# Kernel optimization log

Measured on AMD Instinct MI355X. Metric: run time of the kernel, lower is better.

The kernel has to match this reference:

```python
import jax, jax.numpy as jnp
import numpy as np

B, C_IN, N, T = 16, 2, 207, 12
E = 1863
EMB = 64
HEADS = 8
F_DIM = EMB * T  # 768


def setup_inputs() -> dict:
    key = jax.random.key(0)
    ks = jax.random.split(key, 12)
    s = 0.05
    x = jax.random.normal(ks[0], (B, C_IN, N, T), jnp.float32)
    src = jax.random.randint(ks[1], (E,), 0, N)
    dst = jax.random.randint(ks[2], (E,), 0, N)
    # ensure every node has an incoming edge (self loops in the tail)
    loop = jnp.arange(N)
    src = src.at[-N:].set(loop)
    dst = dst.at[-N:].set(loop)
    Ws = jax.random.normal(ks[3], (EMB, C_IN), jnp.float32) * s
    bs = jnp.zeros((EMB,), jnp.float32)
    Wc = jax.random.normal(ks[4], (EMB, C_IN), jnp.float32) * s
    bc = jnp.zeros((EMB,), jnp.float32)
    W1 = jax.random.normal(ks[5], (F_DIM, HEADS * F_DIM), jnp.float32) * s
    al1 = jax.random.normal(ks[6], (HEADS, F_DIM), jnp.float32) * s
    ar1 = jax.random.normal(ks[7], (HEADS, F_DIM), jnp.float32) * s
    b1 = jnp.zeros((HEADS, F_DIM), jnp.float32)
    W2 = jax.random.normal(ks[8], (F_DIM, HEADS * F_DIM), jnp.float32) * s
    al2 = jax.random.normal(ks[9], (HEADS, F_DIM), jnp.float32) * s
    ar2 = jax.random.normal(ks[10], (HEADS, F_DIM), jnp.float32) * s
    b2 = jnp.zeros((HEADS, F_DIM), jnp.float32)
    return dict(x=x, src=src, dst=dst, Ws=Ws, bs=bs, Wc=Wc, bc=bc,
                W1=W1, al1=al1, ar1=ar1, b1=b1, W2=W2, al2=al2, ar2=ar2, b2=b2)


def _gat_layer(h, W, al, ar, b, src, dst):
    # h: [B, N, F]  (dropout disabled: eval-mode reference)
    feat = (h @ W).reshape(B, N, HEADS, F_DIM)          # [B,N,H,F]
    el = jnp.einsum('bnhf,hf->bnh', feat, al)           # src scores
    er = jnp.einsum('bnhf,hf->bnh', feat, ar)           # dst scores
    e = jax.nn.leaky_relu(el[:, src] + er[:, dst], 0.2)  # [B,E,H]

    def edge_softmax(ev):  # ev: [E,H], softmax over edges sharing a dst node
        m = jax.ops.segment_max(ev, dst, num_segments=N)
        ex = jnp.exp(ev - m[dst])
        denom = jax.ops.segment_sum(ex, dst, num_segments=N)
        return ex / denom[dst]

    alpha = jax.vmap(edge_softmax)(e)                   # [B,E,H]
    msg = alpha[..., None] * feat[:, src]               # [B,E,H,F]
    rst = jax.vmap(lambda m_: jax.ops.segment_sum(m_, dst, num_segments=N))(msg)
    rst = jax.nn.elu(rst + b)                            # bias + F.elu activation
    return rst.mean(axis=2)                              # mean over heads -> [B,N,F]


def reference(x, src, dst, Ws, bs, Wc, bc, W1, al1, ar1, b1, W2, al2, ar2, b2):
    # 1x1 convs == channel matmuls
    x1 = jnp.einsum('bcnt,oc->bont', x, Ws) + bs[None, :, None, None]
    x2 = jax.nn.leaky_relu(jnp.einsum('bcnt,oc->bont', x, Wc) + bc[None, :, None, None], 0.01)
    xm = x1 + x2                                         # [B,EMB,N,T]
    h = xm.transpose(0, 2, 1, 3).reshape(B, N, F_DIM)    # [B,N,768]
    h = _gat_layer(h, W1, al1, ar1, b1, src, dst)
    h = _gat_layer(h, W2, al2, ar2, b2, src, dst)
    gc = h.reshape(B, N, EMB, T).transpose(0, 2, 1, 3)   # [B,EMB,N,T]
    return xm + gc
```

## Files before the change

### kernel.cpp

```cpp
#include <hip/hip_runtime.h>

#define BB 16
#define NNODE 207
#define TTS 12
#define NE 1863
#define NEP2 1920
#define NH 8
#define FD 768
#define HFD 6144
#define MM 3312
#define MP 3328

typedef short bf16x8 __attribute__((ext_vector_type(8)));
typedef float f32x4 __attribute__((ext_vector_type(4)));

typedef __attribute__((address_space(3))) unsigned int lds_u32;
typedef __attribute__((address_space(1))) const unsigned int glb_u32;

__device__ __forceinline__ unsigned short f2b(float f) {
    unsigned int u = __float_as_uint(f);
    u = (u + 0x7FFFu + ((u >> 16) & 1u)) >> 16;
    return (unsigned short)u;
}
__device__ __forceinline__ float b2f(unsigned short b) {
    return __uint_as_float(((unsigned int)b) << 16);
}

__global__ __launch_bounds__(256) void transpose_w(const float* __restrict__ W,
                                                   unsigned short* __restrict__ Wt) {
    __shared__ float tile[64][65];
    const int k0 = blockIdx.x * 64;
    const int n0 = blockIdx.y * 64;
    const int c = threadIdx.x & 63, r0 = threadIdx.x >> 6;
#pragma unroll
    for (int i = 0; i < 16; i++) {
        int r = r0 + i * 4;
        tile[r][c] = W[(size_t)(k0 + r) * HFD + n0 + c];
    }
    __syncthreads();
#pragma unroll
    for (int i = 0; i < 16; i++) {
        int r = r0 + i * 4;
        Wt[(size_t)(n0 + r) * FD + k0 + c] = f2b(tile[c][r]);
    }
}

__global__ __launch_bounds__(256) void prep_h(const float* __restrict__ x,
                                              const float* __restrict__ Ws, const float* __restrict__ bs,
                                              const float* __restrict__ Wc, const float* __restrict__ bc,
                                              float* __restrict__ h0, unsigned short* __restrict__ hbf) {
    const int bn = blockIdx.x;
    const int t = threadIdx.x;
    if (bn >= MM) {
#pragma unroll
        for (int c = 0; c < 3; c++) hbf[(size_t)bn * FD + c * 256 + t] = 0;
        return;
    }
    const int b = bn / NNODE, n = bn % NNODE;
#pragma unroll
    for (int c = 0; c < 3; c++) {
        int idx = c * 256 + t;
        int e = idx / TTS, tt = idx % TTS;
        float x0 = x[((size_t)(b * 2 + 0) * NNODE + n) * TTS + tt];
        float x1 = x[((size_t)(b * 2 + 1) * NNODE + n) * TTS + tt];
        float s1 = Ws[e * 2] * x0 + Ws[e * 2 + 1] * x1 + bs[e];
        float s2 = Wc[e * 2] * x0 + Wc[e * 2 + 1] * x1 + bc[e];
        s2 = s2 > 0.f ? s2 : 0.01f * s2;
        float v = s1 + s2;
        h0[(size_t)bn * FD + idx] = v;
        hbf[(size_t)bn * FD + idx] = f2b(v);
    }
}

#define CSR_EBLK 468
__global__ __launch_bounds__(256) void build_csr3(const int* __restrict__ dst,
                                                  int* __restrict__ ptr, int* __restrict__ cidx) {
    __shared__ int dl[NEP2];
    const int t = threadIdx.x;
    const int wv = t >> 6, lane = t & 63;
    for (int i = t; i < NEP2; i += 256) dl[i] = (i < NE) ? dst[i] : 0x0FFFFFFF;
    __syncthreads();
    if (blockIdx.x < CSR_EBLK) {
        const int e = blockIdx.x * 4 + wv;
        if (e >= NE) return;
        const int d = dl[e];
        int pos = 0;
#pragma unroll
        for (int j = 0; j < 30; j++) {
            int i = lane + j * 64;
            int di = dl[i];
            pos += (int)(di < d) + (int)((i < e) & (di == d));
        }
#pragma unroll
        for (int off = 32; off > 0; off >>= 1) pos += __shfl_down(pos, off);
        if (lane == 0) cidx[pos] = e;
    } else {
        const int n = (blockIdx.x - CSR_EBLK) * 4 + wv;
        if (n > NNODE) return;
        int cnt = 0;
#pragma unroll
        for (int j = 0; j < 30; j++) cnt += (int)(dl[lane + j * 64] < n);
#pragma unroll
        for (int off = 32; off > 0; off >>= 1) cnt += __shfl_down(cnt, off);
        if (lane == 0) ptr[n] = cnt;
    }
}

__global__ __launch_bounds__(256) void gemm_bf16(const unsigned short* __restrict__ A,
                                                 const unsigned short* __restrict__ Bt,
                                                 unsigned short* __restrict__ C) {
    __shared__ __align__(16) unsigned short Alds[128 * 32];
    __shared__ __align__(16) unsigned short Blds[128 * 32];
    const int t = threadIdx.x;
    const int lane = t & 63;
    const int wv = t >> 6;
    const int wr = (wv >> 1) * 64, wc = (wv & 1) * 64;
    const int mt = blockIdx.y * 128, nt = blockIdx.x * 128;
    const int lm = lane & 15;
    const int kb = (lane >> 4) * 8;

    const int r0 = (wv * 2) * 16 + (lane >> 2);
    const int r1 = (wv * 2 + 1) * 16 + (lane >> 2);
    const int cseg = (lane & 3) * 8;
    const size_t aoff0 = (size_t)(mt + r0) * FD + cseg;
    const size_t aoff1 = (size_t)(mt + r1) * FD + cseg;
    const size_t boff0 = (size_t)(nt + r0) * FD + cseg;
    const size_t boff1 = (size_t)(nt + r1) * FD + cseg;
    unsigned short* la0 = Alds + (size_t)(wv * 2) * 512;
    unsigned short* la1 = Alds + (size_t)(wv * 2 + 1) * 512;
    unsigned short* lb0 = Blds + (size_t)(wv * 2) * 512;
    unsigned short* lb1 = Blds + (size_t)(wv * 2 + 1) * 512;

    f32x4 acc[4][4] = {};
    for (int ks = 0; ks < FD; ks += 32) {
        __builtin_amdgcn_global_load_lds((glb_u32*)(A + aoff0 + ks), (lds_u32*)la0, 16, 0, 0);
        __builtin_amdgcn_global_load_lds((glb_u32*)(A + aoff1 + ks), (lds_u32*)la1, 16, 0, 0);
        __builtin_amdgcn_global_load_lds((glb_u32*)(Bt + boff0 + ks), (lds_u32*)lb0, 16, 0, 0);
        __builtin_amdgcn_global_load_lds((glb_u32*)(Bt + boff1 + ks), (lds_u32*)lb1, 16, 0, 0);
        __syncthreads();
        bf16x8 af[4], bfv[4];
#pragma unroll
        for (int i = 0; i < 4; i++) af[i] = *(const bf16x8*)(Alds + (wr + i * 16 + lm) * 32 + kb);
#pragma unroll
        for (int j = 0; j < 4; j++) bfv[j] = *(const bf16x8*)(Blds + (wc + j * 16 + lm) * 32 + kb);
#pragma unroll
        for (int i = 0; i < 4; i++)
#pragma unroll
            for (int j = 0; j < 4; j++)
                acc[i][j] = __builtin_amdgcn_mfma_f32_16x16x32_bf16(af[i], bfv[j], acc[i][j], 0, 0, 0);
        __syncthreads();
    }
    const int rbase = (lane >> 4) * 4;
#pragma unroll
    for (int i = 0; i < 4; i++) {
#pragma unroll
        for (int r = 0; r < 4; r++) {
            int grow = mt + wr + i * 16 + rbase + r;
            if (grow < MM) {
#pragma unroll
                for (int j = 0; j < 4; j++) {
                    int gcol = nt + wc + j * 16 + lm;
                    C[(size_t)grow * HFD + gcol] = f2b(acc[i][j][r]);
                }
            }
        }
    }
}

__global__ __launch_bounds__(256) void eler(const unsigned short* __restrict__ feat,
                                            const float* __restrict__ al, const float* __restrict__ ar,
                                            float* __restrict__ el, float* __restrict__ er) {
    const int p = blockIdx.x * 4 + (threadIdx.x >> 6);
    const int lane = threadIdx.x & 63;
    const int bn = p >> 3, hh = p & 7;
    const size_t base = (size_t)bn * HFD + hh * FD;
    float sl = 0.f, sr = 0.f;
#pragma unroll
    for (int j = 0; j < 12; j++) {
        int f = lane + j * 64;
        float fv = b2f(feat[base + f]);
        sl += fv * al[hh * FD + f];
        sr += fv * ar[hh * FD + f];
    }
#pragma unroll
    for (int off = 32; off > 0; off >>= 1) {
        sl += __shfl_down(sl, off);
        sr += __shfl_down(sr, off);
    }
    if (lane == 0) {
        el[bn * NH + hh] = sl;
        er[bn * NH + hh] = sr;
    }
}

__global__ __launch_bounds__(256) void edge_softmax(const float* __restrict__ el, const float* __restrict__ er,
                                                    const int* __restrict__ cptr, const int* __restrict__ cidx,
                                                    const int* __restrict__ src, float* __restrict__ alp) {
    const int t = blockIdx.x * 256 + threadIdx.x;
    if (t >= BB * NNODE * NH) return;
    const int hh = t & 7;
    const int n = (t >> 3) % NNODE;
    const int b = t / (NNODE * NH);
    const float erv = er[(b * NNODE + n) * NH + hh];
    const int p0 = cptr[n], p1 = cptr[n + 1];
    float m = -1e30f;
    for (int j = p0; j < p1; j++) {
        int e = cidx[j];
        float s = el[(b * NNODE + src[e]) * NH + hh] + erv;
        s = s > 0.f ? s : 0.2f * s;
        m = fmaxf(m, s);
    }
    float den = 0.f;
    for (int j = p0; j < p1; j++) {
        int e = cidx[j];
        float s = el[(b * NNODE + src[e]) * NH + hh] + erv;
        s = s > 0.f ? s : 0.2f * s;
        float ex = expf(s - m);
        den += ex;
        alp[((size_t)b * NE + e) * NH + hh] = ex;
    }
    const float inv = 1.f / den;
    for (int j = p0; j < p1; j++) {
        int e = cidx[j];
        alp[((size_t)b * NE + e) * NH + hh] *= inv;
    }
}

template <int LAST>
__global__ __launch_bounds__(256) void msg_agg(const unsigned short* __restrict__ feat,
                                               const float* __restrict__ alp,
                                               const int* __restrict__ cptr, const int* __restrict__ cidx,
                                               const int* __restrict__ src, const float* __restrict__ bias,
                                               unsigned short* __restrict__ hbf_out,
                                               const float* __restrict__ h0, float* __restrict__ out) {
    __shared__ float rstl[HFD];
    __shared__ int src_l[32];
    __shared__ float alph[32][NH];
    const int bn = (blockIdx.x & 7) * (MM / 8) + (blockIdx.x >> 3);
    const int b = bn / NNODE, n = bn % NNODE;
    const int t = threadIdx.x;
    const int h0i = t / 96, h1i = (256 + t) / 96, h2i = (512 + t) / 96;
    float acc[3][8] = {};
    const int p0 = cptr[n], p1 = cptr[n + 1];
    for (int base = p0; base < p1; base += 32) {
        const int cnt = min(32, p1 - base);
        if (t < cnt) src_l[t] = src[cidx[base + t]];
        {
            int j = t >> 3, hh = t & 7;
            if (j < cnt) alph[j][hh] = alp[((size_t)b * NE + cidx[base + j]) * NH + hh];
        }
        __syncthreads();
        for (int j2 = 0; j2 < cnt; j2++) {
            const size_t srow = (size_t)(b * NNODE + src_l[j2]) * HFD;
            const float a0 = alph[j2][h0i], a1 = alph[j2][h1i], a2 = alph[j2][h2i];
            uint4 pk;
            unsigned int w;
            pk = *(const uint4*)(feat + srow + (size_t)(0 * 256 + t) * 8);
            w = pk.x; acc[0][0] += a0 * b2f((unsigned short)w); acc[0][1] += a0 * b2f((unsigned short)(w >> 16));
            w = pk.y; acc[0][2] += a0 * b2f((unsigned short)w); acc[0][3] += a0 * b2f((unsigned short)(w >> 16));
            w = pk.z; acc[0][4] += a0 * b2f((unsigned short)w); acc[0][5] += a0 * b2f((unsigned short)(w >> 16));
            w = pk.w; acc[0][6] += a0 * b2f((unsigned short)w); acc[0][7] += a0 * b2f((unsigned short)(w >> 16));
            pk = *(const uint4*)(feat + srow + (size_t)(1 * 256 + t) * 8);
            w = pk.x; acc[1][0] += a1 * b2f((unsigned short)w); acc[1][1] += a1 * b2f((unsigned short)(w >> 16));
            w = pk.y; acc[1][2] += a1 * b2f((unsigned short)w); acc[1][3] += a1 * b2f((unsigned short)(w >> 16));
            w = pk.z; acc[1][4] += a1 * b2f((unsigned short)w); acc[1][5] += a1 * b2f((unsigned short)(w >> 16));
            w = pk.w; acc[1][6] += a1 * b2f((unsigned short)w); acc[1][7] += a1 * b2f((unsigned short)(w >> 16));
            pk = *(const uint4*)(feat + srow + (size_t)(2 * 256 + t) * 8);
            w = pk.x; acc[2][0] += a2 * b2f((unsigned short)w); acc[2][1] += a2 * b2f((unsigned short)(w >> 16));
            w = pk.y; acc[2][2] += a2 * b2f((unsigned short)w); acc[2][3] += a2 * b2f((unsigned short)(w >> 16));
            w = pk.z; acc[2][4] += a2 * b2f((unsigned short)w); acc[2][5] += a2 * b2f((unsigned short)(w >> 16));
            w = pk.w; acc[2][6] += a2 * b2f((unsigned short)w); acc[2][7] += a2 * b2f((unsigned short)(w >> 16));
        }
        __syncthreads();
    }
#pragma unroll
    for (int c = 0; c < 3; c++) {
        int v = c * 256 + t;
#pragma unroll
        for (int u = 0; u < 8; u++) rstl[v * 8 + u] = acc[c][u];
    }
    __syncthreads();
#pragma unroll
    for (int q = 0; q < 3; q++) {
        int f = q * 256 + t;
        float val = 0.f;
#pragma unroll
        for (int hh = 0; hh < 8; hh++) {
            float r = rstl[hh * FD + f] + bias[hh * FD + f];
            val += (r > 0.f) ? r : (expf(r) - 1.f);
        }
        val *= 0.125f;
        if (LAST) {
            int e_ = f / TTS, tt_ = f % TTS;
            out[((size_t)(b * 64 + e_) * NNODE + n) * TTS + tt_] = h0[(size_t)bn * FD + f] + val;
        } else {
            hbf_out[(size_t)bn * FD + f] = f2b(val);
        }
    }
}

extern "C" void kernel_launch(void* const* d_in, const int* in_sizes, int n_in,
                              void* d_out, int out_size, void* d_ws, size_t ws_size,
                              hipStream_t stream) {
    const float* x = (const float*)d_in[0];
    const int* src = (const int*)d_in[1];
    const int* dst = (const int*)d_in[2];
    const float* Ws = (const float*)d_in[3];
    const float* bs = (const float*)d_in[4];
    const float* Wc = (const float*)d_in[5];
    const float* bc = (const float*)d_in[6];
    const float* W1 = (const float*)d_in[7];
    const float* al1 = (const float*)d_in[8];
    const float* ar1 = (const float*)d_in[9];
    const float* b1 = (const float*)d_in[10];
    const float* W2 = (const float*)d_in[11];
    const float* al2 = (const float*)d_in[12];
    const float* ar2 = (const float*)d_in[13];
    const float* b2 = (const float*)d_in[14];
    float* out = (float*)d_out;

    char* w = (char*)d_ws;
    size_t off = 0;
    auto alloc = [&](size_t bytes) -> void* {
        void* p = w + off;
        off = (off + bytes + 255) & ~(size_t)255;
        return p;
    };
    float* h0 = (float*)alloc((size_t)MM * FD * 4);
    unsigned short* hbf = (unsigned short*)alloc((size_t)MP * FD * 2);
    unsigned short* Wt = (unsigned short*)alloc((size_t)HFD * FD * 2);
    unsigned short* feat = (unsigned short*)alloc((size_t)MM * HFD * 2);
    float* el = (float*)alloc((size_t)MM * NH * 4);
    float* er = (float*)alloc((size_t)MM * NH * 4);
    float* alp = (float*)alloc((size_t)BB * NE * NH * 4);
    int* cptr = (int*)alloc((NNODE + 1) * 4);
    int* cidx = (int*)alloc(NE * 4);

    transpose_w<<<dim3(12, 96), 256, 0, stream>>>(W1, Wt);
    prep_h<<<MP, 256, 0, stream>>>(x, Ws, bs, Wc, bc, h0, hbf);
    build_csr3<<<CSR_EBLK + 52, 256, 0, stream>>>(dst, cptr, cidx);

    gemm_bf16<<<dim3(48, 26), 256, 0, stream>>>(hbf, Wt, feat);
    transpose_w<<<dim3(12, 96), 256, 0, stream>>>(W2, Wt);
    eler<<<6624, 256, 0, stream>>>(feat, al1, ar1, el, er);
    edge_softmax<<<104, 256, 0, stream>>>(el, er, cptr, cidx, src, alp);
    msg_agg<0><<<MM, 256, 0, stream>>>(feat, alp, cptr, cidx, src, b1, hbf, nullptr, nullptr);

    gemm_bf16<<<dim3(48, 26), 256, 0, stream>>>(hbf, Wt, feat);
    eler<<<6624, 256, 0, stream>>>(feat, al2, ar2, el, er);
    edge_softmax<<<104, 256, 0, stream>>>(el, er, cptr, cidx, src, alp);
    msg_agg<1><<<MM, 256, 0, stream>>>(feat, alp, cptr, cidx, src, b2, nullptr, h0, out);
}
```

Baseline: 238.9 us.

## Fuse attention score projections into GEMM epilogue, swizzle LDS, remap tiles per XCD

Computes the per-head el/er dot products directly from the fp32 GEMM accumulators in the epilogue, writing per-64-column partial sums that a small reduce kernel combines. This removes the separate eler kernel, which re-read the whole bf16 feat tensor. The change also XOR-swizzles the LDS layout to cut bank conflicts and remaps the 1D block index so each XCD works on a contiguous tile region for better L2 locality. In exchange it adds epilogue shuffles and partial-sum buffers. The scores are now taken from fp32 accumulators rather than bf16-rounded features, so numerics shift slightly.

Measured after the change: 258.4 us. 8.2% more time.

```diff
diff --git a/kernel.cpp b/kernel.cpp
--- a/kernel.cpp
+++ b/kernel.cpp
@@ -108,20 +108,29 @@
 
 __global__ __launch_bounds__(256) void gemm_bf16(const unsigned short* __restrict__ A,
                                                  const unsigned short* __restrict__ Bt,
-                                                 unsigned short* __restrict__ C) {
+                                                 unsigned short* __restrict__ C,
+                                                 const float* __restrict__ al,
+                                                 const float* __restrict__ ar,
+                                                 float* __restrict__ pel,
+                                                 float* __restrict__ per) {
     __shared__ __align__(16) unsigned short Alds[128 * 32];
     __shared__ __align__(16) unsigned short Blds[128 * 32];
     const int t = threadIdx.x;
     const int lane = t & 63;
     const int wv = t >> 6;
     const int wr = (wv >> 1) * 64, wc = (wv & 1) * 64;
-    const int mt = blockIdx.y * 128, nt = blockIdx.x * 128;
+    const int id = blockIdx.x;
+    const int xcd = id & 7, k = id >> 3;
+    const int tr = (xcd & 1) * 13 + k / 12;
+    const int tc = (xcd >> 1) * 12 + k % 12;
+    const int mt = tr * 128, nt = tc * 128;
     const int lm = lane & 15;
-    const int kb = (lane >> 4) * 8;
+    const int rsw = (lm >> 1) & 3;
+    const int s4 = lane >> 4;
 
     const int r0 = (wv * 2) * 16 + (lane >> 2);
     const int r1 = (wv * 2 + 1) * 16 + (lane >> 2);
-    const int cseg = (lane & 3) * 8;
+    const int cseg = (((lane & 3) ^ ((lane >> 3) & 3)) * 8);
     const size_t aoff0 = (size_t)(mt + r0) * FD + cseg;
     const size_t aoff1 = (size_t)(mt + r1) * FD + cseg;
     const size_t boff0 = (size_t)(nt + r0) * FD + cseg;
@@ -140,9 +149,11 @@
         __syncthreads();
         bf16x8 af[4], bfv[4];
 #pragma unroll
-        for (int i = 0; i < 4; i++) af[i] = *(const bf16x8*)(Alds + (wr + i * 16 + lm) * 32 + kb);
-#pragma unroll
-        for (int j = 0; j < 4; j++) bfv[j] = *(const bf16x8*)(Blds + (wc + j * 16 + lm) * 32 + kb);
+        for (int i = 0; i < 4; i++)
+            af[i] = *(const bf16x8*)(Alds + (wr + i * 16 + lm) * 32 + (s4 ^ rsw) * 8);
+#pragma unroll
+        for (int j = 0; j < 4; j++)
+            bfv[j] = *(const bf16x8*)(Blds + (wc + j * 16 + lm) * 32 + (s4 ^ rsw) * 8);
 #pragma unroll
         for (int i = 0; i < 4; i++)
 #pragma unroll
@@ -150,7 +161,7 @@
                 acc[i][j] = __builtin_amdgcn_mfma_f32_16x16x32_bf16(af[i], bfv[j], acc[i][j], 0, 0, 0);
         __syncthreads();
     }
-    const int rbase = (lane >> 4) * 4;
+    const int rbase = s4 * 4;
 #pragma unroll
     for (int i = 0; i < 4; i++) {
 #pragma unroll
@@ -165,32 +176,52 @@
             }
         }
     }
-}
-
-__global__ __launch_bounds__(256) void eler(const unsigned short* __restrict__ feat,
-                                            const float* __restrict__ al, const float* __restrict__ ar,
-                                            float* __restrict__ el, float* __restrict__ er) {
-    const int p = blockIdx.x * 4 + (threadIdx.x >> 6);
-    const int lane = threadIdx.x & 63;
-    const int bn = p >> 3, hh = p & 7;
-    const size_t base = (size_t)bn * HFD + hh * FD;
-    float sl = 0.f, sr = 0.f;
+    float alv[4], arv[4];
+#pragma unroll
+    for (int j = 0; j < 4; j++) {
+        int gcol = nt + wc + j * 16 + lm;
+        alv[j] = al[gcol];
+        arv[j] = ar[gcol];
+    }
+    const int pidx = tc * 2 + (wc >> 6);
+#pragma unroll
+    for (int i = 0; i < 4; i++) {
+#pragma unroll
+        for (int r = 0; r < 4; r++) {
+            float pl = acc[i][0][r] * alv[0] + acc[i][1][r] * alv[1] +
+                       acc[i][2][r] * alv[2] + acc[i][3][r] * alv[3];
+            float pr = acc[i][0][r] * arv[0] + acc[i][1][r] * arv[1] +
+                       acc[i][2][r] * arv[2] + acc[i][3][r] * arv[3];
+#pragma unroll
+            for (int m = 1; m < 16; m <<= 1) {
+                pl += __shfl_xor(pl, m);
+                pr += __shfl_xor(pr, m);
+            }
+            if (lm == 0) {
+                int grow = mt + wr + i * 16 + rbase + r;
+                if (grow < MM) {
+                    pel[(size_t)pidx * MP + grow] = pl;
+                    per[(size_t)pidx * MP + grow] = pr;
+                }
+            }
+        }
+    }
+}
+
+__global__ __launch_bounds__(256) void reduce_eler(const float* __restrict__ pel,
+                                                   const float* __restrict__ per,
+                                                   float* __restrict__ el, float* __restrict__ er) {
+    const int idx = blockIdx.x * 256 + threadIdx.x;
+    if (idx >= MM * NH) return;
+    const int h = idx / MM, bn = idx % MM;
+    float s = 0.f, u = 0.f;
 #pragma unroll
     for (int j = 0; j < 12; j++) {
-        int f = lane + j * 64;
-        float fv = b2f(feat[base + f]);
-        sl += fv * al[hh * FD + f];
-        sr += fv * ar[hh * FD + f];
-    }
-#pragma unroll
-    for (int off = 32; off > 0; off >>= 1) {
-        sl += __shfl_down(sl, off);
-        sr += __shfl_down(sr, off);
-    }
-    if (lane == 0) {
-        el[bn * NH + hh] = sl;
-        er[bn * NH + hh] = sr;
-    }
+        s += pel[(size_t)(h * 12 + j) * MP + bn];
+        u += per[(size_t)(h * 12 + j) * MP + bn];
+    }
+    el[bn * NH + h] = s;
+    er[bn * NH + h] = u;
 }
 
 __global__ __launch_bounds__(256) void edge_softmax(const float* __restrict__ el, const float* __restrict__ er,
@@ -335,19 +366,21 @@
     float* alp = (float*)alloc((size_t)BB * NE * NH * 4);
     int* cptr = (int*)alloc((NNODE + 1) * 4);
     int* cidx = (int*)alloc(NE * 4);
+    float* pel = (float*)alloc((size_t)96 * MP * 4);
+    float* per = (float*)alloc((size_t)96 * MP * 4);
 
     transpose_w<<<dim3(12, 96), 256, 0, stream>>>(W1, Wt);
     prep_h<<<MP, 256, 0, stream>>>(x, Ws, bs, Wc, bc, h0, hbf);
     build_csr3<<<CSR_EBLK + 52, 256, 0, stream>>>(dst, cptr, cidx);
 
-    gemm_bf16<<<dim3(48, 26), 256, 0, stream>>>(hbf, Wt, feat);
+    gemm_bf16<<<1248, 256, 0, stream>>>(hbf, Wt, feat, al1, ar1, pel, per);
     transpose_w<<<dim3(12, 96), 256, 0, stream>>>(W2, Wt);
-    eler<<<6624, 256, 0, stream>>>(feat, al1, ar1, el, er);
+    reduce_eler<<<104, 256, 0, stream>>>(pel, per, el, er);
     edge_softmax<<<104, 256, 0, stream>>>(el, er, cptr, cidx, src, alp);
     msg_agg<0><<<MM, 256, 0, stream>>>(feat, alp, cptr, cidx, src, b1, hbf, nullptr, nullptr);
 
-    gemm_bf16<<<dim3(48, 26), 256, 0, stream>>>(hbf, Wt, feat);
-    eler<<<6624, 256, 0, stream>>>(feat, al2, ar2, el, er);
+    gemm_bf16<<<1248, 256, 0, stream>>>(hbf, Wt, feat, al2, ar2, pel, per);
+    reduce_eler<<<104, 256, 0, stream>>>(pel, per, el, er);
     edge_softmax<<<104, 256, 0, stream>>>(el, er, cptr, cidx, src, alp);
     msg_agg<1><<<MM, 256, 0, stream>>>(feat, alp, cptr, cidx, src, b2, nullptr, h0, out);
 }
```

## Double-buffer GEMM LDS tiles and XOR-swizzle to avoid bank conflicts

Applied to the files above, without the earlier changes.

The bf16 GEMM now keeps two LDS buffers for the A and B tiles and prefetches the next K-slice with global_load_lds while the MFMA loop runs on the current slice. This drops one barrier per iteration and lets global loads overlap with compute. The global source column segment and the LDS read offset are XOR-swizzled per row to reduce LDS bank conflicts on the fragment reads. LDS use doubles, and correctness now depends on the write and read swizzles matching.

Result: no change. 242.7 us (+1.6%).

```diff
diff --git a/kernel.cpp b/kernel.cpp
--- a/kernel.cpp
+++ b/kernel.cpp
@@ -109,48 +109,72 @@
 __global__ __launch_bounds__(256) void gemm_bf16(const unsigned short* __restrict__ A,
                                                  const unsigned short* __restrict__ Bt,
                                                  unsigned short* __restrict__ C) {
-    __shared__ __align__(16) unsigned short Alds[128 * 32];
-    __shared__ __align__(16) unsigned short Blds[128 * 32];
+    __shared__ __align__(16) unsigned short Alds[2][128 * 32];
+    __shared__ __align__(16) unsigned short Blds[2][128 * 32];
     const int t = threadIdx.x;
     const int lane = t & 63;
     const int wv = t >> 6;
     const int wr = (wv >> 1) * 64, wc = (wv & 1) * 64;
     const int mt = blockIdx.y * 128, nt = blockIdx.x * 128;
     const int lm = lane & 15;
-    const int kb = (lane >> 4) * 8;
+    const int rsw = (lm >> 1) & 3;
+    const int s4 = lane >> 4;
+    const int rdoff = (s4 ^ rsw) * 8;
 
     const int r0 = (wv * 2) * 16 + (lane >> 2);
     const int r1 = (wv * 2 + 1) * 16 + (lane >> 2);
-    const int cseg = (lane & 3) * 8;
-    const size_t aoff0 = (size_t)(mt + r0) * FD + cseg;
-    const size_t aoff1 = (size_t)(mt + r1) * FD + cseg;
-    const size_t boff0 = (size_t)(nt + r0) * FD + cseg;
-    const size_t boff1 = (size_t)(nt + r1) * FD + cseg;
-    unsigned short* la0 = Alds + (size_t)(wv * 2) * 512;
-    unsigned short* la1 = Alds + (size_t)(wv * 2 + 1) * 512;
-    unsigned short* lb0 = Blds + (size_t)(wv * 2) * 512;
-    unsigned short* lb1 = Blds + (size_t)(wv * 2 + 1) * 512;
+    const int cseg = (((lane & 3) ^ ((lane >> 3) & 3)) * 8);
+    const unsigned short* ap0 = A + (size_t)(mt + r0) * FD + cseg;
+    const unsigned short* ap1 = A + (size_t)(mt + r1) * FD + cseg;
+    const unsigned short* bp0 = Bt + (size_t)(nt + r0) * FD + cseg;
+    const unsigned short* bp1 = Bt + (size_t)(nt + r1) * FD + cseg;
+    const int ldoff0 = (wv * 2) * 512;
+    const int ldoff1 = (wv * 2 + 1) * 512;
 
     f32x4 acc[4][4] = {};
-    for (int ks = 0; ks < FD; ks += 32) {
-        __builtin_amdgcn_global_load_lds((glb_u32*)(A + aoff0 + ks), (lds_u32*)la0, 16, 0, 0);
-        __builtin_amdgcn_global_load_lds((glb_u32*)(A + aoff1 + ks), (lds_u32*)la1, 16, 0, 0);
-        __builtin_amdgcn_global_load_lds((glb_u32*)(Bt + boff0 + ks), (lds_u32*)lb0, 16, 0, 0);
-        __builtin_amdgcn_global_load_lds((glb_u32*)(Bt + boff1 + ks), (lds_u32*)lb1, 16, 0, 0);
-        __syncthreads();
+    __builtin_amdgcn_global_load_lds((glb_u32*)(ap0), (lds_u32*)(Alds[0] + ldoff0), 16, 0, 0);
+    __builtin_amdgcn_global_load_lds((glb_u32*)(ap1), (lds_u32*)(Alds[0] + ldoff1), 16, 0, 0);
+    __builtin_amdgcn_global_load_lds((glb_u32*)(bp0), (lds_u32*)(Blds[0] + ldoff0), 16, 0, 0);
+    __builtin_amdgcn_global_load_lds((glb_u32*)(bp1), (lds_u32*)(Blds[0] + ldoff1), 16, 0, 0);
+    __syncthreads();
+
+    int cur = 0;
+#pragma unroll 1
+    for (int ks = 32; ks < FD; ks += 32) {
+        __builtin_amdgcn_global_load_lds((glb_u32*)(ap0 + ks), (lds_u32*)(Alds[cur ^ 1] + ldoff0), 16, 0, 0);
+        __builtin_amdgcn_global_load_lds((glb_u32*)(ap1 + ks), (lds_u32*)(Alds[cur ^ 1] + ldoff1), 16, 0, 0);
+        __builtin_amdgcn_global_load_lds((glb_u32*)(bp0 + ks), (lds_u32*)(Blds[cur ^ 1] + ldoff0), 16, 0, 0);
+        __builtin_amdgcn_global_load_lds((glb_u32*)(bp1 + ks), (lds_u32*)(Blds[cur ^ 1] + ldoff1), 16, 0, 0);
         bf16x8 af[4], bfv[4];
 #pragma unroll
-        for (int i = 0; i < 4; i++) af[i] = *(const bf16x8*)(Alds + (wr + i * 16 + lm) * 32 + kb);
-#pragma unroll
-        for (int j = 0; j < 4; j++) bfv[j] = *(const bf16x8*)(Blds + (wc + j * 16 + lm) * 32 + kb);
+        for (int i = 0; i < 4; i++)
+            af[i] = *(const bf16x8*)(Alds[cur] + (wr + i * 16 + lm) * 32 + rdoff);
+#pragma unroll
+        for (int j = 0; j < 4; j++)
+            bfv[j] = *(const bf16x8*)(Blds[cur] + (wc + j * 16 + lm) * 32 + rdoff);
 #pragma unroll
         for (int i = 0; i < 4; i++)
 #pragma unroll
             for (int j = 0; j < 4; j++)
                 acc[i][j] = __builtin_amdgcn_mfma_f32_16x16x32_bf16(af[i], bfv[j], acc[i][j], 0, 0, 0);
         __syncthreads();
-    }
-    const int rbase = (lane >> 4) * 4;
+        cur ^= 1;
+    }
+    {
+        bf16x8 af[4], bfv[4];
+#pragma unroll
+        for (int i = 0; i < 4; i++)
+            af[i] = *(const bf16x8*)(Alds[cur] + (wr + i * 16 + lm) * 32 + rdoff);
+#pragma unroll
+        for (int j = 0; j < 4; j++)
+            bfv[j] = *(const bf16x8*)(Blds[cur] + (wc + j * 16 + lm) * 32 + rdoff);
+#pragma unroll
+        for (int i = 0; i < 4; i++)
+#pragma unroll
+            for (int j = 0; j < 4; j++)
+                acc[i][j] = __builtin_amdgcn_mfma_f32_16x16x32_bf16(af[i], bfv[j], acc[i][j], 0, 0, 0);
+    }
+    const int rbase = s4 * 4;
 #pragma unroll
     for (int i = 0; i < 4; i++) {
 #pragma unroll
```

## Fold attention vectors into weights and compute el/er from layer inputs

Applied to the files above, without the earlier changes.

Precomputes W·al and W·ar per head so the attention scores el/er can be computed directly from the 768-wide layer input. That work is fused into prep_h and msg_agg<0>, which removes the separate eler pass over the large bf16 feat tensor. Both weight transposes now run in one launch into two buffers, and the GEMM's LDS layout gets an XOR swizzle to reduce bank conflicts. It costs a small extra precompute kernel and extra workspace, and el/er are now computed in fp32 from h rather than from bf16-rounded feat, so the numerics change slightly.

New measurement: 301.2 us. 26.1% more time.

```diff
diff --git a/kernel.cpp b/kernel.cpp
--- a/kernel.cpp
+++ b/kernel.cpp
@@ -26,9 +26,38 @@
     return __uint_as_float(((unsigned int)b) << 16);
 }
 
-__global__ __launch_bounds__(256) void transpose_w(const float* __restrict__ W,
-                                                   unsigned short* __restrict__ Wt) {
+__global__ __launch_bounds__(256) void prep_wlr(const float* __restrict__ W1,
+                                                const float* __restrict__ al1, const float* __restrict__ ar1,
+                                                const float* __restrict__ W2,
+                                                const float* __restrict__ al2, const float* __restrict__ ar2,
+                                                float* __restrict__ wlr) {
+    const int d = blockIdx.x * 256 + threadIdx.x;
+    const int which = d / 6144;
+    const int r = d % 6144;
+    const int k = r >> 3, hh = r & 7;
+    const float* W = which ? W2 : W1;
+    const float* al = which ? al2 : al1;
+    const float* ar = which ? ar2 : ar1;
+    const float4* wp = (const float4*)(W + (size_t)k * HFD + hh * FD);
+    const float4* ap = (const float4*)(al + hh * FD);
+    const float4* rp = (const float4*)(ar + hh * FD);
+    float sl = 0.f, sr = 0.f;
+    for (int j = 0; j < 192; j++) {
+        float4 w = wp[j], a = ap[j], b = rp[j];
+        sl += w.x * a.x + w.y * a.y + w.z * a.z + w.w * a.w;
+        sr += w.x * b.x + w.y * b.y + w.z * b.z + w.w * b.w;
+    }
+    wlr[(size_t)which * 12288 + 0 + hh * FD + k] = sl;
+    wlr[(size_t)which * 12288 + 6144 + hh * FD + k] = sr;
+}
+
+__global__ __launch_bounds__(256) void transpose_w2(const float* __restrict__ W1,
+                                                    const float* __restrict__ W2,
+                                                    unsigned short* __restrict__ Wt1,
+                                                    unsigned short* __restrict__ Wt2) {
     __shared__ float tile[64][65];
+    const float* W = blockIdx.z ? W2 : W1;
+    unsigned short* Wt = blockIdx.z ? Wt2 : Wt1;
     const int k0 = blockIdx.x * 64;
     const int n0 = blockIdx.y * 64;
     const int c = threadIdx.x & 63, r0 = threadIdx.x >> 6;
@@ -48,7 +77,10 @@
 __global__ __launch_bounds__(256) void prep_h(const float* __restrict__ x,
                                               const float* __restrict__ Ws, const float* __restrict__ bs,
                                               const float* __restrict__ Wc, const float* __restrict__ bc,
-                                              float* __restrict__ h0, unsigned short* __restrict__ hbf) {
+                                              const float* __restrict__ wl, const float* __restrict__ wr,
+                                              float* __restrict__ h0, unsigned short* __restrict__ hbf,
+                                              float* __restrict__ el, float* __restrict__ er) {
+    __shared__ float redl[4][8], redr[4][8];
     const int bn = blockIdx.x;
     const int t = threadIdx.x;
     if (bn >= MM) {
@@ -57,6 +89,7 @@
         return;
     }
     const int b = bn / NNODE, n = bn % NNODE;
+    float pl[8] = {}, pr[8] = {};
 #pragma unroll
     for (int c = 0; c < 3; c++) {
         int idx = c * 256 + t;
@@ -69,6 +102,27 @@
         float v = s1 + s2;
         h0[(size_t)bn * FD + idx] = v;
         hbf[(size_t)bn * FD + idx] = f2b(v);
+#pragma unroll
+        for (int hh = 0; hh < 8; hh++) {
+            pl[hh] += v * wl[hh * FD + idx];
+            pr[hh] += v * wr[hh * FD + idx];
+        }
+    }
+    const int wv = t >> 6, lane = t & 63;
+#pragma unroll
+    for (int hh = 0; hh < 8; hh++) {
+        float a = pl[hh], c2 = pr[hh];
+#pragma unroll
+        for (int off = 32; off > 0; off >>= 1) {
+            a += __shfl_down(a, off);
+            c2 += __shfl_down(c2, off);
+        }
+        if (lane == 0) { redl[wv][hh] = a; redr[wv][hh] = c2; }
+    }
+    __syncthreads();
+    if (t < 8) {
+        el[bn * NH + t] = redl[0][t] + redl[1][t] + redl[2][t] + redl[3][t];
+        er[bn * NH + t] = redr[0][t] + redr[1][t] + redr[2][t] + redr[3][t];
     }
 }
 
@@ -117,11 +171,13 @@
     const int wr = (wv >> 1) * 64, wc = (wv & 1) * 64;
     const int mt = blockIdx.y * 128, nt = blockIdx.x * 128;
     const int lm = lane & 15;
-    const int kb = (lane >> 4) * 8;
+    const int rsw = (lm >> 1) & 3;
+    const int s4 = lane >> 4;
+    const int rdoff = (s4 ^ rsw) * 8;
 
     const int r0 = (wv * 2) * 16 + (lane >> 2);
     const int r1 = (wv * 2 + 1) * 16 + (lane >> 2);
-    const int cseg = (lane & 3) * 8;
+    const int cseg = (((lane & 3) ^ ((lane >> 3) & 3)) * 8);
     const size_t aoff0 = (size_t)(mt + r0) * FD + cseg;
     const size_t aoff1 = (size_t)(mt + r1) * FD + cseg;
     const size_t boff0 = (size_t)(nt + r0) * FD + cseg;
@@ -140,9 +196,11 @@
         __syncthreads();
         bf16x8 af[4], bfv[4];
 #pragma unroll
-        for (int i = 0; i < 4; i++) af[i] = *(const bf16x8*)(Alds + (wr + i * 16 + lm) * 32 + kb);
-#pragma unroll
-        for (int j = 0; j < 4; j++) bfv[j] = *(const bf16x8*)(Blds + (wc + j * 16 + lm) * 32 + kb);
+        for (int i = 0; i < 4; i++)
+            af[i] = *(const bf16x8*)(Alds + (wr + i * 16 + lm) * 32 + rdoff);
+#pragma unroll
+        for (int j = 0; j < 4; j++)
+            bfv[j] = *(const bf16x8*)(Blds + (wc + j * 16 + lm) * 32 + rdoff);
 #pragma unroll
         for (int i = 0; i < 4; i++)
 #pragma unroll
@@ -150,7 +208,7 @@
                 acc[i][j] = __builtin_amdgcn_mfma_f32_16x16x32_bf16(af[i], bfv[j], acc[i][j], 0, 0, 0);
         __syncthreads();
     }
-    const int rbase = (lane >> 4) * 4;
+    const int rbase = s4 * 4;
 #pragma unroll
     for (int i = 0; i < 4; i++) {
 #pragma unroll
@@ -164,32 +222,6 @@
                 }
             }
         }
-    }
-}
-
-__global__ __launch_bounds__(256) void eler(const unsigned short* __restrict__ feat,
-                                            const float* __restrict__ al, const float* __restrict__ ar,
-                                            float* __restrict__ el, float* __restrict__ er) {
-    const int p = blockIdx.x * 4 + (threadIdx.x >> 6);
-    const int lane = threadIdx.x & 63;
-    const int bn = p >> 3, hh = p & 7;
-    const size_t base = (size_t)bn * HFD + hh * FD;
-    float sl = 0.f, sr = 0.f;
-#pragma unroll
-    for (int j = 0; j < 12; j++) {
-        int f = lane + j * 64;
-        float fv = b2f(feat[base + f]);
-        sl += fv * al[hh * FD + f];
-        sr += fv * ar[hh * FD + f];
-    }
-#pragma unroll
-    for (int off = 32; off > 0; off >>= 1) {
-        sl += __shfl_down(sl, off);
-        sr += __shfl_down(sr, off);
-    }
-    if (lane == 0) {
-        el[bn * NH + hh] = sl;
-        er[bn * NH + hh] = sr;
     }
 }
 
@@ -232,10 +264,13 @@
                                                const int* __restrict__ cptr, const int* __restrict__ cidx,
                                                const int* __restrict__ src, const float* __restrict__ bias,
                                                unsigned short* __restrict__ hbf_out,
+                                               const float* __restrict__ wl, const float* __restrict__ wr,
+                                               float* __restrict__ el, float* __restrict__ er,
                                                const float* __restrict__ h0, float* __restrict__ out) {
     __shared__ float rstl[HFD];
     __shared__ int src_l[32];
     __shared__ float alph[32][NH];
+    __shared__ float redl[4][8], redr[4][8];
     const int bn = (blockIdx.x & 7) * (MM / 8) + (blockIdx.x >> 3);
     const int b = bn / NNODE, n = bn % NNODE;
     const int t = threadIdx.x;
@@ -280,6 +315,7 @@
         for (int u = 0; u < 8; u++) rstl[v * 8 + u] = acc[c][u];
     }
     __syncthreads();
+    float pl[8] = {}, pr[8] = {};
 #pragma unroll
     for (int q = 0; q < 3; q++) {
         int f = q * 256 + t;
@@ -295,6 +331,29 @@
             out[((size_t)(b * 64 + e_) * NNODE + n) * TTS + tt_] = h0[(size_t)bn * FD + f] + val;
         } else {
             hbf_out[(size_t)bn * FD + f] = f2b(val);
+#pragma unroll
+            for (int hh = 0; hh < 8; hh++) {
+                pl[hh] += val * wl[hh * FD + f];
+                pr[hh] += val * wr[hh * FD + f];
+            }
+        }
+    }
+    if (!LAST) {
+        const int wv = t >> 6, lane = t & 63;
+#pragma unroll
+        for (int hh = 0; hh < 8; hh++) {
+            float a = pl[hh], c2 = pr[hh];
+#pragma unroll
+            for (int off = 32; off > 0; off >>= 1) {
+                a += __shfl_down(a, off);
+                c2 += __shfl_down(c2, off);
+            }
+            if (lane == 0) { redl[wv][hh] = a; redr[wv][hh] = c2; }
+        }
+        __syncthreads();
+        if (t < 8) {
+            el[bn * NH + t] = redl[0][t] + redl[1][t] + redl[2][t] + redl[3][t];
+            er[bn * NH + t] = redr[0][t] + redr[1][t] + redr[2][t] + redr[3][t];
         }
     }
 }
@@ -328,26 +387,27 @@
     };
     float* h0 = (float*)alloc((size_t)MM * FD * 4);
     unsigned short* hbf = (unsigned short*)alloc((size_t)MP * FD * 2);
-    unsigned short* Wt = (unsigned short*)alloc((size_t)HFD * FD * 2);
+    unsigned short* Wt1 = (unsigned short*)alloc((size_t)HFD * FD * 2);
+    unsigned short* Wt2 = (unsigned short*)alloc((size_t)HFD * FD * 2);
     unsigned short* feat = (unsigned short*)alloc((size_t)MM * HFD * 2);
     float* el = (float*)alloc((size_t)MM * NH * 4);
     float* er = (float*)alloc((size_t)MM * NH * 4);
     float* alp = (float*)alloc((size_t)BB * NE * NH * 4);
     int* cptr = (int*)alloc((NNODE + 1) * 4);
     int* cidx = (int*)alloc(NE * 4);
-
-    transpose_w<<<dim3(12, 96), 256, 0, stream>>>(W1, Wt);
-    prep_h<<<MP, 256, 0, stream>>>(x, Ws, bs, Wc, bc, h0, hbf);
+    float* wlr = (float*)alloc((size_t)4 * 6144 * 4);
+    float* wl1 = wlr, * wr1 = wlr + 6144, * wl2 = wlr + 12288, * wr2 = wlr + 18432;
+
+    prep_wlr<<<48, 256, 0, stream>>>(W1, al1, ar1, W2, al2, ar2, wlr);
+    transpose_w2<<<dim3(12, 96, 2), 256, 0, stream>>>(W1, W2, Wt1, Wt2);
+    prep_h<<<MP, 256, 0, stream>>>(x, Ws, bs, Wc, bc, wl1, wr1, h0, hbf, el, er);
     build_csr3<<<CSR_EBLK + 52, 256, 0, stream>>>(dst, cptr, cidx);
 
-    gemm_bf16<<<dim3(48, 26), 256, 0, stream>>>(hbf, Wt, feat);
-    transpose_w<<<dim3(12, 96), 256, 0, stream>>>(W2, Wt);
-    eler<<<6624, 256, 0, stream>>>(feat, al1, ar1, el, er);
     edge_softmax<<<104, 256, 0, stream>>>(el, er, cptr, cidx, src, alp);
-    msg_agg<0><<<MM, 256, 0, stream>>>(feat, alp, cptr, cidx, src, b1, hbf, nullptr, nullptr);
-
-    gemm_bf16<<<dim3(48, 26), 256, 0, stream>>>(hbf, Wt, feat);
-    eler<<<6624, 256, 0, stream>>>(feat, al2, ar2, el, er);
+    gemm_bf16<<<dim3(48, 26), 256, 0, stream>>>(hbf, Wt1, feat);
+    msg_agg<0><<<MM, 256, 0, stream>>>(feat, alp, cptr, cidx, src, b1, hbf, wl2, wr2, el, er, nullptr, nullptr);
+
     edge_softmax<<<104, 256, 0, stream>>>(el, er, cptr, cidx, src, alp);
-    msg_agg<1><<<MM, 256, 0, stream>>>(feat, alp, cptr, cidx, src, b2, nullptr, h0, out);
-}
+    gemm_bf16<<<dim3(48, 26), 256, 0, stream>>>(hbf, Wt2, feat);
+    msg_agg<1><<<MM, 256, 0, stream>>>(feat, alp, cptr, cidx, src, b2, nullptr, nullptr, nullptr, nullptr, nullptr, h0, out);
+}
```
